# Performance work log

Hardware: AMD Instinct MI355X
Metric: run time of the kernel (lower is better)

Reference implementation:

```python
import jax, jax.numpy as jnp
import numpy as np

N_NODES = 100000

def _sage_conv(x, src, dst, W_l, b_l, W_r):
    # PyG SAGEConv (aggr='mean'): out = lin_l(mean_{j in N(i)} x_j) + lin_r(x_i)
    msg = x[src]                                             # [E, d] gather
    agg = jax.ops.segment_sum(msg, dst, num_segments=N_NODES)  # [N, d]
    deg = jax.ops.segment_sum(jnp.ones((src.shape[0],), x.dtype), dst,
                              num_segments=N_NODES)          # [N]
    mean = agg / jnp.maximum(deg, 1.0)[:, None]
    return mean @ W_l + b_l + x @ W_r

def setup_inputs() -> dict:
    key = jax.random.key(0)
    ks = jax.random.split(key, 8)
    d_in, d_hid, d_out = 128, 128, 64
    E = 1_600_000
    x = jax.random.normal(ks[0], (N_NODES, d_in), dtype=jnp.float32)
    edge_index = jax.random.randint(ks[1], (2, E), 0, N_NODES, dtype=jnp.int64)
    s1 = 1.0 / np.sqrt(d_in)
    s2 = 1.0 / np.sqrt(d_hid)
    return {
        "x": x,
        "W1_l": jax.random.uniform(ks[2], (d_in, d_hid), jnp.float32, -s1, s1),
        "b1":   jnp.zeros((d_hid,), jnp.float32),
        "W1_r": jax.random.uniform(ks[3], (d_in, d_hid), jnp.float32, -s1, s1),
        "W2_l": jax.random.uniform(ks[4], (d_hid, d_out), jnp.float32, -s2, s2),
        "b2":   jnp.zeros((d_out,), jnp.float32),
        "W2_r": jax.random.uniform(ks[5], (d_hid, d_out), jnp.float32, -s2, s2),
        "edge_index": edge_index,
    }

def reference(x, W1_l, b1, W1_r, W2_l, b2, W2_r, edge_index):
    src, dst = edge_index[0], edge_index[1]
    h = _sage_conv(x, src, dst, W1_l, b1, W1_r)
    h = jax.nn.relu(h)
    # dropout is identity in eval mode (p=0.5 train-only); omitted for determinism
    out = _sage_conv(h, src, dst, W2_l, b2, W2_r)
    return out
```

## Files before the change

### kernel.cpp

```cpp
#include <hip/hip_runtime.h>
#include <hip/hip_bf16.h>
#include <cstdint>


typedef __bf16 bf16x8 __attribute__((ext_vector_type(8)));
typedef float f32x4 __attribute__((ext_vector_type(4)));
typedef float f32x2 __attribute__((ext_vector_type(2)));

#define MAXBUCK 800
#define CAP 2560
#define MAXEPT 16
#define P2B 512
#define P2E (MAXEPT * 256)
#define HSTRIDE 136

__device__ __forceinline__ unsigned short f2bf(float f) {
    union { float f; unsigned int u; } v; v.f = f;
    unsigned int u = v.u;
    unsigned int r = ((u >> 16) & 1u) + 0x7fffu;
    return (unsigned short)((u + r) >> 16);
}

__device__ __forceinline__ f32x2 up2(unsigned int u) {
    uint2 t; t.x = u << 16; t.y = u & 0xffff0000u;
    return __builtin_bit_cast(f32x2, t);
}
__device__ __forceinline__ void accp(const uint4& v, f32x2* a) {
    a[0] += up2(v.x);
    a[1] += up2(v.y);
    a[2] += up2(v.z);
    a[3] += up2(v.w);
}
__device__ __forceinline__ void accpw(const uint4& v, float w, f32x2* a) {
    a[0] += up2(v.x) * w;
    a[1] += up2(v.y) * w;
    a[2] += up2(v.z) * w;
    a[3] += up2(v.w) * w;
}

__device__ __forceinline__ int edge_val(const int* ei32, const long long* ei64,
                                        int is64, size_t idx) {
    return is64 ? (int)ei64[idx] : ei32[idx];
}

__global__ __launch_bounds__(256) void fused_front(const float* __restrict__ x,
                                                   unsigned short* __restrict__ xb,
                                                   long long n8, int ncvt,
                                                   const float* __restrict__ W1l,
                                                   const float* __restrict__ W1r,
                                                   uint4* __restrict__ w1frag,
                                                   const float* __restrict__ W2l,
                                                   const float* __restrict__ W2r,
                                                   uint4* __restrict__ w2frag,
                                                   const int* __restrict__ ei32,
                                                   const long long* __restrict__ ei64,
                                                   int E, int ept, int nbuck,
                                                   int n_nodes,
                                                   int* __restrict__ bucket_pos,
                                                   unsigned* __restrict__ ebuf) {
    __shared__ int lhist[MAXBUCK];
    __shared__ int lexcl[MAXBUCK];
    __shared__ int gbase[MAXBUCK];
    __shared__ int part[256];
    __shared__ unsigned estage[P2E];
    __shared__ unsigned short bstage[P2E];
    int b = blockIdx.x;
    int t = threadIdx.x;
    if (b < P2B) {
        for (int i = t; i < nbuck; i += 256) lhist[i] = 0;
        __syncthreads();
        int is64;
        {
            int ok = 1;
            for (int i = 0; i < 8; ++i) {
                long long v = ei64[i];
                if (v < 0 || v >= n_nodes) ok = 0;
            }
            is64 = ok;
        }
        int base_e = b * (ept * 256);
        unsigned ed[MAXEPT];
        int bidx[MAXEPT];
        int slot[MAXEPT];
#pragma unroll 4
        for (int i = 0; i < ept; ++i) {
            int e = base_e + i * 256 + t;
            if (e < E) {
                int s = edge_val(ei32, ei64, is64, (size_t)e);
                int d = edge_val(ei32, ei64, is64, (size_t)E + e);
                ed[i] = ((unsigned)s << 7) | (unsigned)(d & 127);
                bidx[i] = d >> 7;
                slot[i] = atomicAdd(&lhist[d >> 7], 1);
            } else {
                slot[i] = -1;
            }
        }
        __syncthreads();
        int base4 = t * 4;
        int c0 = (base4 + 0 < nbuck) ? lhist[base4 + 0] : 0;
        int c1 = (base4 + 1 < nbuck) ? lhist[base4 + 1] : 0;
        int c2 = (base4 + 2 < nbuck) ? lhist[base4 + 2] : 0;
        int c3 = (base4 + 3 < nbuck) ? lhist[base4 + 3] : 0;
        int lsum = c0 + c1 + c2 + c3;
        part[t] = lsum;
        __syncthreads();
        for (int o = 1; o < 256; o <<= 1) {
            int xv = 0;
            if (t >= o) xv = part[t - o];
            __syncthreads();
            if (t >= o) part[t] += xv;
            __syncthreads();
        }
        {
            int run = part[t] - lsum;
            if (base4 + 0 < nbuck) { lexcl[base4 + 0] = run; run += c0; }
            if (base4 + 1 < nbuck) { lexcl[base4 + 1] = run; run += c1; }
            if (base4 + 2 < nbuck) { lexcl[base4 + 2] = run; run += c2; }
            if (base4 + 3 < nbuck) { lexcl[base4 + 3] = run; run += c3; }
        }
        for (int i = t; i < nbuck; i += 256) {
            int c = lhist[i];
            gbase[i] = c ? atomicAdd(&bucket_pos[i], c) : 0;
        }
        __syncthreads();
#pragma unroll 4
        for (int i = 0; i < ept; ++i) {
            if (slot[i] >= 0) {
                int pos = lexcl[bidx[i]] + slot[i];
                estage[pos] = ed[i];
                bstage[pos] = (unsigned short)bidx[i];
            }
        }
        __syncthreads();
        int m_blk = E - base_e;
        if (m_blk < 0) m_blk = 0;
        if (m_blk > ept * 256) m_blk = ept * 256;
        for (int s = t; s < m_blk; s += 256) {
            int bb = bstage[s];
            int pos = gbase[bb] + (s - lexcl[bb]);
            if (pos < CAP) ebuf[(size_t)bb * CAP + pos] = estage[s];
        }
        return;
    }
    int cb = b - P2B;
    if (cb < ncvt) {
        long long i = (long long)cb * 256 + t;
        if (i >= n8) return;
        const float4* p = (const float4*)(x + i * 8);
        float4 a = p[0], c = p[1];
        uint4 o;
        o.x = (unsigned)f2bf(a.x) | ((unsigned)f2bf(a.y) << 16);
        o.y = (unsigned)f2bf(a.z) | ((unsigned)f2bf(a.w) << 16);
        o.z = (unsigned)f2bf(c.x) | ((unsigned)f2bf(c.y) << 16);
        o.w = (unsigned)f2bf(c.z) | ((unsigned)f2bf(c.w) << 16);
        ((uint4*)(xb))[i] = o;
        return;
    }
    if (cb < ncvt + 16) {
        int tid = (cb - ncvt) * 256 + t;
        int fi = tid >> 6, lane = tid & 63;
        int ct = fi >> 3, ks = fi & 7;
        int k0 = ks * 32 + (lane >> 4) * 8;
        int n = ct * 16 + (lane & 15);
        unsigned short e[8];
#pragma unroll
        for (int j = 0; j < 8; ++j) {
            int k = k0 + j;
            float v = (k < 128) ? W1l[k * 128 + n] : W1r[(k - 128) * 128 + n];
            e[j] = f2bf(v);
        }
        uint4 o;
        o.x = (unsigned)e[0] | ((unsigned)e[1] << 16);
        o.y = (unsigned)e[2] | ((unsigned)e[3] << 16);
        o.z = (unsigned)e[4] | ((unsigned)e[5] << 16);
        o.w = (unsigned)e[6] | ((unsigned)e[7] << 16);
        w1frag[tid] = o;
        return;
    }
    int tid = (cb - ncvt - 16) * 256 + t;
    if (tid >= 2048) return;
    int fi = tid >> 6, lane = tid & 63;
    int ct = fi >> 2, ks = fi & 3;
    int k0 = ks * 32 + (lane >> 4) * 8;
    int n = ct * 16 + (lane & 15);
    unsigned short e[8];
#pragma unroll
    for (int j = 0; j < 8; ++j) {
        int k = k0 + j;
        float v = (n < 64) ? W2l[k * 64 + n] : W2r[k * 64 + (n - 64)];
        e[j] = f2bf(v);
    }
    uint4 o;
    o.x = (unsigned)e[0] | ((unsigned)e[1] << 16);
    o.y = (unsigned)e[2] | ((unsigned)e[3] << 16);
    o.z = (unsigned)e[4] | ((unsigned)e[5] << 16);
    o.w = (unsigned)e[6] | ((unsigned)e[7] << 16);
    w2frag[tid] = o;
}

__global__ __launch_bounds__(256) void pass3_finalize(const unsigned* __restrict__ ebuf,
                                                      const int* __restrict__ bucket_pos,
                                                      int nbuck, int N,
                                                      int2* __restrict__ startcnt,
                                                      int* __restrict__ csr) {
    __shared__ int lcnt[128];
    __shared__ int lexcl[128];
    __shared__ int sc[128];
    int b = blockIdx.x;
    int t = threadIdx.x;
    int d0 = b << 7;
    int nb = N - d0; if (nb > 128) nb = 128;
    int m = bucket_pos[b]; if (m > CAP) m = CAP;
    const unsigned* eb = ebuf + (size_t)b * CAP;

    if (t < 128) lcnt[t] = 0;
    __syncthreads();
    for (int j = t; j < m; j += 256) {
        atomicAdd(&lcnt[eb[j] & 127u], 1);
    }
    __syncthreads();
    int v = 0;
    if (t < 128) { v = lcnt[t]; sc[t] = v; }
    __syncthreads();
    for (int o = 1; o < 128; o <<= 1) {
        int x = 0;
        if (t < 128 && t >= o) x = sc[t - o];
        __syncthreads();
        if (t < 128 && t >= o) sc[t] += x;
        __syncthreads();
    }
    if (t < 128) {
        int excl = sc[t] - v;
        lexcl[t] = excl;
        if (t < nb) startcnt[d0 + t] = make_int2(b * CAP + excl, v);
        lcnt[t] = 0;
    }
    __syncthreads();
    for (int j = t; j < m; j += 256) {
        unsigned ed = eb[j];
        int li = (int)(ed & 127u);
        int slot = atomicAdd(&lcnt[li], 1);
        csr[b * CAP + lexcl[li] + slot] = (int)(ed >> 7);
    }
}

__global__ __launch_bounds__(1024, 8) void agg16_gemm(const unsigned short* __restrict__ Xb,
                                                      const int2* __restrict__ startcnt,
                                                      const int* __restrict__ csr,
                                                      const uint4* __restrict__ w1frag,
                                                      const uint4* __restrict__ w2frag,
                                                      const float* __restrict__ b1,
                                                      const float* __restrict__ b2,
                                                      unsigned short* __restrict__ z2,
                                                      float* __restrict__ outw2,
                                                      int n_nodes) {
    __shared__ unsigned short ms[16 * HSTRIDE];
    __shared__ unsigned short xs[16 * HSTRIDE];
    __shared__ unsigned short hsb[16 * HSTRIDE];
    const int t = threadIdx.x;
    const int wid = t >> 6;
    const int lane = t & 63;
    const int quad = lane >> 4, l16 = lane & 15;

    {
        int node = blockIdx.x * 16 + wid;
        if (node >= n_nodes) node = n_nodes - 1;
        if (quad == 0) {
            *(uint4*)(xs + wid * HSTRIDE + l16 * 8) =
                ((const uint4*)(Xb + (size_t)node * 128))[l16];
        }
        int2 sc2 = startcnt[node];
        int s0 = sc2.x, deg = sc2.y, s1 = s0 + deg;
        f32x2 A0[4], A1[4];
#pragma unroll
        for (int k = 0; k < 4; ++k) { A0[k] = (f32x2){0.f, 0.f}; A1[k] = (f32x2){0.f, 0.f}; }
        int j = s0;
        for (; j + 8 <= s1; j += 8) {
            int p0 = csr[j + quad];
            int p1 = csr[j + 4 + quad];
            uint4 v0 = ((const uint4*)(Xb + (size_t)p0 * 128))[l16];
            uint4 v1 = ((const uint4*)(Xb + (size_t)p1 * 128))[l16];
            accp(v0, A0);
            accp(v1, A1);
        }
        if (j + 4 <= s1) {
            int p = csr[j + quad];
            uint4 v = ((const uint4*)(Xb + (size_t)p * 128))[l16];
            accp(v, A0);
            j += 4;
        }
        if (j < s1) {
            int jj = j + quad;
            int p = csr[(jj < s1) ? jj : (s1 - 1)];
            float w = (jj < s1) ? 1.0f : 0.0f;
            uint4 v = ((const uint4*)(Xb + (size_t)p * 128))[l16];
            accpw(v, w, A1);
        }
        float r[8];
#pragma unroll
        for (int k = 0; k < 4; ++k) {
            f32x2 s = A0[k] + A1[k];
            r[2 * k] = s.x;
            r[2 * k + 1] = s.y;
        }
#pragma unroll
        for (int k = 0; k < 8; ++k) r[k] += __shfl(r[k], lane ^ 16);
#pragma unroll
        for (int k = 0; k < 8; ++k) r[k] += __shfl(r[k], lane ^ 32);
        float inv = (deg > 0) ? 1.0f / (float)deg : 0.0f;
        if (quad == 0) {
            uint4 o;
            o.x = (unsigned)f2bf(r[0] * inv) | ((unsigned)f2bf(r[1] * inv) << 16);
            o.y = (unsigned)f2bf(r[2] * inv) | ((unsigned)f2bf(r[3] * inv) << 16);
            o.z = (unsigned)f2bf(r[4] * inv) | ((unsigned)f2bf(r[5] * inv) << 16);
            o.w = (unsigned)f2bf(r[6] * inv) | ((unsigned)f2bf(r[7] * inv) << 16);
            *(uint4*)(ms + wid * HSTRIDE + l16 * 8) = o;
        }
    }
    __syncthreads();

    if (wid < 8) {
        bf16x8 af[8];
#pragma unroll
        for (int ks = 0; ks < 4; ++ks) {
            af[ks] = __builtin_bit_cast(bf16x8,
                *(const uint4*)(ms + l16 * HSTRIDE + ks * 32 + quad * 8));
            af[ks + 4] = __builtin_bit_cast(bf16x8,
                *(const uint4*)(xs + l16 * HSTRIDE + ks * 32 + quad * 8));
        }
        const uint4* w1p = w1frag + lane;
        f32x4 a0 = (f32x4){0.f, 0.f, 0.f, 0.f};
#pragma unroll
        for (int ks = 0; ks < 8; ++ks) {
            uint4 wc = w1p[(wid * 8 + ks) * 64];
            a0 = __builtin_amdgcn_mfma_f32_16x16x32_bf16(
                af[ks], __builtin_bit_cast(bf16x8, wc), a0, 0, 0, 0);
        }
        int col = wid * 16 + l16;
        float bb = b1[col];
#pragma unroll
        for (int r = 0; r < 4; ++r) {
            hsb[(quad * 4 + r) * HSTRIDE + col] = f2bf(fmaxf(a0[r] + bb, 0.f));
        }
    }
    __syncthreads();

    if (wid >= 8) {
        int ct = wid - 8;
        bf16x8 af2[4];
#pragma unroll
        for (int ks = 0; ks < 4; ++ks) {
            af2[ks] = __builtin_bit_cast(bf16x8,
                *(const uint4*)(hsb + l16 * HSTRIDE + ks * 32 + quad * 8));
        }
        const uint4* w2p = w2frag + lane;
        f32x4 a0 = (f32x4){0.f, 0.f, 0.f, 0.f};
#pragma unroll
        for (int ks = 0; ks < 4; ++ks) {
            uint4 wc2 = w2p[(ct * 4 + ks) * 64];
            a0 = __builtin_amdgcn_mfma_f32_16x16x32_bf16(
                af2[ks], __builtin_bit_cast(bf16x8, wc2), a0, 0, 0, 0);
        }
        int col = ct * 16 + l16;
#pragma unroll
        for (int r = 0; r < 4; ++r) {
            int orow = blockIdx.x * 16 + quad * 4 + r;
            if (orow < n_nodes) {
                if (col < 64) {
                    z2[(size_t)orow * 64 + col] = f2bf(a0[r]);
                } else {
                    outw2[(size_t)orow * 64 + (col - 64)] = a0[r] + b2[col - 64];
                }
            }
        }
    }
}

__global__ __launch_bounds__(256) void agg_mean64_bf_ep(const unsigned short* __restrict__ Zb,
                                                        const int2* __restrict__ startcnt,
                                                        const int* __restrict__ csr,
                                                        float* __restrict__ out,
                                                        int n_nodes) {
    int node = blockIdx.x * 8 + (threadIdx.x >> 5);
    if (node >= n_nodes) return;
    int lane = threadIdx.x & 63;
    int hl = lane & 31;
    int oct4 = hl >> 3;
    int l8 = hl & 7;
    int2 sc2 = startcnt[node];
    int s0 = sc2.x, deg = sc2.y, s1 = s0 + deg;
    f32x2 A0[4], A1[4];
#pragma unroll
    for (int k = 0; k < 4; ++k) { A0[k] = (f32x2){0.f, 0.f}; A1[k] = (f32x2){0.f, 0.f}; }
    int j = s0;
    for (; j + 8 <= s1; j += 8) {
        int p0 = csr[j + oct4];
        int p1 = csr[j + 4 + oct4];
        uint4 v0 = ((const uint4*)(Zb + (size_t)p0 * 64))[l8];
        uint4 v1 = ((const uint4*)(Zb + (size_t)p1 * 64))[l8];
        accp(v0, A0);
        accp(v1, A1);
    }
    if (j + 4 <= s1) {
        int p = csr[j + oct4];
        uint4 v = ((const uint4*)(Zb + (size_t)p * 64))[l8];
        accp(v, A0);
        j += 4;
    }
    if (j < s1) {
        int jj = j + oct4;
        int p = csr[(jj < s1) ? jj : (s1 - 1)];
        float w = (jj < s1) ? 1.0f : 0.0f;
        uint4 v = ((const uint4*)(Zb + (size_t)p * 64))[l8];
        accpw(v, w, A1);
    }
    float r[8];
#pragma unroll
    for (int k = 0; k < 4; ++k) {
        f32x2 s = A0[k] + A1[k];
        r[2 * k] = s.x;
        r[2 * k + 1] = s.y;
    }
#pragma unroll
    for (int k = 0; k < 8; ++k) r[k] += __shfl(r[k], lane ^ 8);
#pragma unroll
    for (int k = 0; k < 8; ++k) r[k] += __shfl(r[k], lane ^ 16);
    float inv = (deg > 0) ? 1.0f / (float)deg : 0.0f;
    if (oct4 == 0) {
        float4* op = (float4*)(out + (size_t)node * 64 + l8 * 8);
        float4 w0 = op[0], w1 = op[1];
        float4 o0, o1;
        o0.x = r[0] * inv + w0.x; o0.y = r[1] * inv + w0.y;
        o0.z = r[2] * inv + w0.z; o0.w = r[3] * inv + w0.w;
        o1.x = r[4] * inv + w1.x; o1.y = r[5] * inv + w1.y;
        o1.z = r[6] * inv + w1.z; o1.w = r[7] * inv + w1.w;
        op[0] = o0; op[1] = o1;
    }
}

extern "C" void kernel_launch(void* const* d_in, const int* in_sizes, int n_in,
                              void* d_out, int out_size, void* d_ws, size_t ws_size,
                              hipStream_t stream) {
    const float* x    = (const float*)d_in[0];
    const float* W1_l = (const float*)d_in[1];
    const float* b1   = (const float*)d_in[2];
    const float* W1_r = (const float*)d_in[3];
    const float* W2_l = (const float*)d_in[4];
    const float* b2   = (const float*)d_in[5];
    const float* W2_r = (const float*)d_in[6];
    const void*  ei   = d_in[7];
    float* out = (float*)d_out;

    const int N = in_sizes[0] / 128;
    const int E = in_sizes[7] / 2;
    const int nbuck = (N + 127) >> 7;

    uintptr_t base = (uintptr_t)d_ws;
    int* bucket_pos = (int*)(base + 64);
    int2* startcnt = (int2*)(base + 8192);
    int* csr = (int*)(((uintptr_t)(startcnt + N) + 255) & ~(uintptr_t)255);
    uintptr_t p = ((uintptr_t)(csr + (size_t)nbuck * CAP) + 255) & ~(uintptr_t)255;
    unsigned short* xb    = (unsigned short*)p; p += (size_t)N * 128 * 2;
    unsigned short* ebr   = (unsigned short*)p; p += (size_t)N * 128 * 2;
    unsigned short* hbr   = (unsigned short*)p; p += (size_t)N * 128 * 2;
    uint4* w1frag = (uint4*)p; p += 4096 * 16;
    uint4* w2frag = (uint4*)p; p += 2048 * 16;
    unsigned* ebuf = (unsigned*)ebr;
    unsigned short* z2 = hbr;

    const int* ei32 = (const int*)ei;
    const long long* ei64 = (const long long*)ei;

    hipMemsetAsync(bucket_pos, 0, (size_t)nbuck * sizeof(int), stream);

    long long n8 = (long long)N * 128 / 8;
    int ncvt = (int)((n8 + 255) / 256);
    int ept = (E + P2B * 256 - 1) / (P2B * 256);

    fused_front<<<P2B + ncvt + 24, 256, 0, stream>>>(
        x, xb, n8, ncvt, W1_l, W1_r, w1frag, W2_l, W2_r, w2frag,
        ei32, ei64, E, ept, nbuck, N, bucket_pos, ebuf);

    pass3_finalize<<<nbuck, 256, 0, stream>>>(ebuf, bucket_pos, nbuck, N,
                                              startcnt, csr);

    int gblocks = (N + 15) / 16;
    agg16_gemm<<<gblocks, 1024, 0, stream>>>(xb, startcnt, csr,
                                             w1frag, w2frag, b1, b2,
                                             z2, out, N);

    int a64blocks = (N + 7) / 8;
    agg_mean64_bf_ep<<<a64blocks, 256, 0, stream>>>(z2, startcnt, csr, out, N);
}
```

Measured before the change: 272.6 us.

## Sort nodes by degree so each aggregation block handles similar-degree nodes

Builds a degree histogram in the CSR finalize pass, then adds a counting-sort kernel that produces a node permutation ordered by (clamped) in-degree. The fused aggregate+GEMM kernel processes nodes in permuted order and scatters its outputs through the permutation. The aim is to cut load imbalance between waves in a 16-node block, since the block waits for its highest-degree node. In exchange it adds an extra kernel launch, an indirection, scattered output writes, and poorer locality for the node's own feature rows.

```diff
diff --git a/kernel.cpp b/kernel.cpp
--- a/kernel.cpp
+++ b/kernel.cpp
@@ -13,6 +13,7 @@
 #define P2B 512
 #define P2E (MAXEPT * 256)
 #define HSTRIDE 136
+#define NBIN 64
 
 __device__ __forceinline__ unsigned short f2bf(float f) {
     union { float f; unsigned int u; } v; v.f = f;
@@ -202,10 +203,12 @@
                                                       const int* __restrict__ bucket_pos,
                                                       int nbuck, int N,
                                                       int2* __restrict__ startcnt,
-                                                      int* __restrict__ csr) {
+                                                      int* __restrict__ csr,
+                                                      int* __restrict__ dhist) {
     __shared__ int lcnt[128];
     __shared__ int lexcl[128];
     __shared__ int sc[128];
+    __shared__ int ldh[NBIN];
     int b = blockIdx.x;
     int t = threadIdx.x;
     int d0 = b << 7;
@@ -214,6 +217,7 @@
     const unsigned* eb = ebuf + (size_t)b * CAP;
 
     if (t < 128) lcnt[t] = 0;
+    if (t < NBIN) ldh[t] = 0;
     __syncthreads();
     for (int j = t; j < m; j += 256) {
         atomicAdd(&lcnt[eb[j] & 127u], 1);
@@ -232,10 +236,17 @@
     if (t < 128) {
         int excl = sc[t] - v;
         lexcl[t] = excl;
-        if (t < nb) startcnt[d0 + t] = make_int2(b * CAP + excl, v);
+        if (t < nb) {
+            startcnt[d0 + t] = make_int2(b * CAP + excl, v);
+            atomicAdd(&ldh[(v > 63) ? 63 : v], 1);
+        }
         lcnt[t] = 0;
     }
     __syncthreads();
+    if (t < NBIN) {
+        int c = ldh[t];
+        if (c) atomicAdd(&dhist[t], c);
+    }
     for (int j = t; j < m; j += 256) {
         unsigned ed = eb[j];
         int li = (int)(ed & 127u);
@@ -244,9 +255,57 @@
     }
 }
 
+__global__ __launch_bounds__(256) void build_perm(const int2* __restrict__ startcnt,
+                                                  const int* __restrict__ dhist,
+                                                  int* __restrict__ dcur,
+                                                  int* __restrict__ nodeperm,
+                                                  int N) {
+    __shared__ int lh[NBIN];
+    __shared__ int gb[NBIN];
+    __shared__ int sc64[NBIN];
+    int t = threadIdx.x;
+    if (t < NBIN) lh[t] = 0;
+    __syncthreads();
+    int n0 = blockIdx.x * 1024;
+    int dloc[4], sloc[4];
+#pragma unroll
+    for (int i = 0; i < 4; ++i) {
+        int n = n0 + i * 256 + t;
+        if (n < N) {
+            int d = startcnt[n].y; if (d > 63) d = 63;
+            dloc[i] = d;
+            sloc[i] = atomicAdd(&lh[d], 1);
+        } else sloc[i] = -1;
+    }
+    int dh0 = 0;
+    if (t < NBIN) { dh0 = dhist[t]; sc64[t] = dh0; }
+    __syncthreads();
+    for (int o = 1; o < NBIN; o <<= 1) {
+        int xv = 0;
+        if (t < NBIN && t >= o) xv = sc64[t - o];
+        __syncthreads();
+        if (t < NBIN && t >= o) sc64[t] += xv;
+        __syncthreads();
+    }
+    if (t < NBIN) {
+        int dbase = sc64[t] - dh0;
+        int c = lh[t];
+        gb[t] = dbase + (c ? atomicAdd(&dcur[t], c) : 0);
+    }
+    __syncthreads();
+#pragma unroll
+    for (int i = 0; i < 4; ++i) {
+        if (sloc[i] >= 0) {
+            int n = n0 + i * 256 + t;
+            nodeperm[gb[dloc[i]] + sloc[i]] = n;
+        }
+    }
+}
+
 __global__ __launch_bounds__(1024, 8) void agg16_gemm(const unsigned short* __restrict__ Xb,
                                                       const int2* __restrict__ startcnt,
                                                       const int* __restrict__ csr,
+                                                      const int* __restrict__ nodeperm,
                                                       const uint4* __restrict__ w1frag,
                                                       const uint4* __restrict__ w2frag,
                                                       const float* __restrict__ b1,
@@ -257,14 +316,17 @@
     __shared__ unsigned short ms[16 * HSTRIDE];
     __shared__ unsigned short xs[16 * HSTRIDE];
     __shared__ unsigned short hsb[16 * HSTRIDE];
+    __shared__ int pn[16];
     const int t = threadIdx.x;
     const int wid = t >> 6;
     const int lane = t & 63;
     const int quad = lane >> 4, l16 = lane & 15;
 
     {
-        int node = blockIdx.x * 16 + wid;
-        if (node >= n_nodes) node = n_nodes - 1;
+        int slot = blockIdx.x * 16 + wid;
+        if (slot >= n_nodes) slot = n_nodes - 1;
+        int node = nodeperm[slot];
+        if (lane == 0) pn[wid] = node;
         if (quad == 0) {
             *(uint4*)(xs + wid * HSTRIDE + l16 * 8) =
                 ((const uint4*)(Xb + (size_t)node * 128))[l16];
@@ -364,13 +426,11 @@
         int col = ct * 16 + l16;
 #pragma unroll
         for (int r = 0; r < 4; ++r) {
-            int orow = blockIdx.x * 16 + quad * 4 + r;
-            if (orow < n_nodes) {
-                if (col < 64) {
-                    z2[(size_t)orow * 64 + col] = f2bf(a0[r]);
-                } else {
-                    outw2[(size_t)orow * 64 + (col - 64)] = a0[r] + b2[col - 64];
-                }
+            int orow = pn[quad * 4 + r];
+            if (col < 64) {
+                z2[(size_t)orow * 64 + col] = f2bf(a0[r]);
+            } else {
+                outw2[(size_t)orow * 64 + (col - 64)] = a0[r] + b2[col - 64];
             }
         }
     }
@@ -457,6 +517,8 @@
 
     uintptr_t base = (uintptr_t)d_ws;
     int* bucket_pos = (int*)(base + 64);
+    int* dhist = (int*)(base + 4096);
+    int* dcur  = (int*)(base + 4352);
     int2* startcnt = (int2*)(base + 8192);
     int* csr = (int*)(((uintptr_t)(startcnt + N) + 255) & ~(uintptr_t)255);
     uintptr_t p = ((uintptr_t)(csr + (size_t)nbuck * CAP) + 255) & ~(uintptr_t)255;
@@ -467,11 +529,12 @@
     uint4* w2frag = (uint4*)p; p += 2048 * 16;
     unsigned* ebuf = (unsigned*)ebr;
     unsigned short* z2 = hbr;
+    int* nodeperm = (int*)(hbr + (size_t)N * 64);
 
     const int* ei32 = (const int*)ei;
     const long long* ei64 = (const long long*)ei;
 
-    hipMemsetAsync(bucket_pos, 0, (size_t)nbuck * sizeof(int), stream);
+    hipMemsetAsync((void*)base, 0, 8192, stream);
 
     long long n8 = (long long)N * 128 / 8;
     int ncvt = (int)((n8 + 255) / 256);
@@ -482,10 +545,13 @@
         ei32, ei64, E, ept, nbuck, N, bucket_pos, ebuf);
 
     pass3_finalize<<<nbuck, 256, 0, stream>>>(ebuf, bucket_pos, nbuck, N,
-                                              startcnt, csr);
+                                              startcnt, csr, dhist);
+
+    int pblocks = (N + 1023) / 1024;
+    build_perm<<<pblocks, 256, 0, stream>>>(startcnt, dhist, dcur, nodeperm, N);
 
     int gblocks = (N + 15) / 16;
-    agg16_gemm<<<gblocks, 1024, 0, stream>>>(xb, startcnt, csr,
+    agg16_gemm<<<gblocks, 1024, 0, stream>>>(xb, startcnt, csr, nodeperm,
                                              w1frag, w2frag, b1, b2,
                                              z2, out, N);
 
```

Measured after the change: 289.5 us. +6.2%, slower.
